# Kernel optimization log

Measured on AMD Instinct MI355X. Metric: run time of the kernel, lower is better.

The kernel has to match this reference:

```python
import jax, jax.numpy as jnp
import numpy as np

D_MODEL = 1024
N_HEADS = 16
D_HEAD = D_MODEL // N_HEADS


def setup_inputs() -> dict:
    key = jax.random.key(0)
    ks = jax.random.split(key, 7)
    x = jax.random.normal(ks[0], (1, 4096, D_MODEL), dtype=jnp.float32)
    # torch Linear default init ~ U(-1/sqrt(fan_in), 1/sqrt(fan_in)); small randn is fine for a reference
    Wqkv = jax.random.normal(ks[1], (3 * D_MODEL, D_MODEL), dtype=jnp.float32) * (1.0 / np.sqrt(D_MODEL))
    bqkv = jax.random.normal(ks[2], (3 * D_MODEL,), dtype=jnp.float32) * 0.01
    Wo = jax.random.normal(ks[3], (D_MODEL, D_MODEL), dtype=jnp.float32) * (1.0 / np.sqrt(D_MODEL))
    bo = jax.random.normal(ks[4], (D_MODEL,), dtype=jnp.float32) * 0.01
    wq = jnp.ones((D_HEAD,), dtype=jnp.float32)
    wk = jnp.ones((D_HEAD,), dtype=jnp.float32)
    return {"x": x, "Wqkv": Wqkv, "bqkv": bqkv, "Wo": Wo, "bo": bo, "wq": wq, "wk": wk}


def _rmsnorm(x, w):
    # matches RMSNormRef: mean of squares over last dim, eps added to mean before sqrt
    xf = x.astype(jnp.float32)
    rms = jnp.mean(xf * xf, axis=-1, keepdims=True)
    return (xf / jnp.sqrt(rms + 1e-6) * w.astype(jnp.float32)).astype(x.dtype)


def reference(x, Wqkv, bqkv, Wo, bo, wq, wk):
    b, s, d = x.shape
    qkv = x @ Wqkv.T + bqkv                       # [b, s, 3d]
    q, k, v = jnp.split(qkv, 3, axis=-1)
    q = q.reshape(b, s, N_HEADS, D_HEAD)
    k = k.reshape(b, s, N_HEADS, D_HEAD)
    v = v.reshape(b, s, N_HEADS, D_HEAD)
    q = _rmsnorm(q, wq)
    k = _rmsnorm(k, wk)
    # NOTE: original applies NO 1/sqrt(d_head) scaling and NO causal mask
    qf = q.astype(jnp.float32)
    kf = k.astype(jnp.float32)
    vf = v.astype(jnp.float32)
    attn = jnp.einsum('bqhd,bkhd->bhqk', qf, kf)  # [b, h, s, s] fp32 scores
    attn = jax.nn.softmax(attn, axis=-1)
    z = jnp.einsum('bhqk,bkhd->bqhd', attn, vf).astype(x.dtype)
    z = z.reshape(b, s, d)
    return z @ Wo.T + bo
```

## Files before the change

### kernel.cpp

```cpp
#include <hip/hip_runtime.h>
#include <hip/hip_bf16.h>

typedef __bf16 bf16;
typedef bf16 bf16x8 __attribute__((ext_vector_type(8)));
typedef bf16 bf16x4 __attribute__((ext_vector_type(4)));
typedef float f32x4 __attribute__((ext_vector_type(4)));
typedef float f32x16 __attribute__((ext_vector_type(16)));
typedef unsigned int u32;
typedef u32 u32x4 __attribute__((ext_vector_type(4)));

static constexpr int SEQ    = 4096;
static constexpr int DMODEL = 1024;
static constexpr int NHEADS = 16;
static constexpr int DHEAD  = 64;
static constexpr int QKV3   = 3 * DMODEL;
static constexpr float SMAX = 64.0f;

__device__ inline void gld16(const bf16* g, bf16* l) {
    __builtin_amdgcn_global_load_lds(
        (const __attribute__((address_space(1))) void*)g,
        (__attribute__((address_space(3))) void*)l, 16, 0, 0);
}

__device__ inline bf16x8 load8(const float* src) {
    float4 a = *(const float4*)(src);
    float4 b = *(const float4*)(src + 4);
    bf16x8 r;
    r[0] = (bf16)a.x; r[1] = (bf16)a.y; r[2] = (bf16)a.z; r[3] = (bf16)a.w;
    r[4] = (bf16)b.x; r[5] = (bf16)b.y; r[6] = (bf16)b.z; r[7] = (bf16)b.w;
    return r;
}

__device__ inline f32x16 zero16() {
    f32x16 r;
#pragma unroll
    for (int i = 0; i < 16; ++i) r[i] = 0.f;
    return r;
}

static constexpr size_t NX = (size_t)SEQ * DMODEL;
static constexpr size_t NW = (size_t)QKV3 * DMODEL;
static constexpr size_t NO = (size_t)DMODEL * DMODEL;

__global__ __launch_bounds__(256)
void cvt_all(const float* __restrict__ x, const float* __restrict__ Wqkv,
             const float* __restrict__ Wo, bf16* __restrict__ outbase) {
    const size_t e = ((size_t)blockIdx.x * 256 + threadIdx.x) * 8;
    const float* src;
    if (e < NX)            src = x + e;
    else if (e < NX + NW)  src = Wqkv + (e - NX);
    else                   src = Wo + (e - NX - NW);
    *(bf16x8*)(outbase + e) = load8(src);
}

__global__ __launch_bounds__(256)
void gemm_qkv(const bf16* __restrict__ A, const bf16* __restrict__ W,
              const float* __restrict__ bias, const float* __restrict__ wq,
              const float* __restrict__ wk, bf16* __restrict__ qkv,
              bf16* __restrict__ Vt) {
    __shared__ __align__(16) bf16 As[128 * 32];
    __shared__ __align__(16) bf16 Ws[128 * 32];
    const int tid  = threadIdx.x;
    const int wave = tid >> 6;
    const int ll   = tid & 15;
    const int quad = (tid & 63) >> 4;
    const int wm   = (wave >> 1) * 64;
    const int wn   = (wave & 1) * 64;
    const int m0 = blockIdx.y * 128;
    const int n0 = blockIdx.x * 128;

    f32x4 acc[4][4];
#pragma unroll
    for (int i = 0; i < 4; ++i)
#pragma unroll
        for (int j = 0; j < 4; ++j) acc[i][j] = (f32x4){0.f, 0.f, 0.f, 0.f};

    for (int k0 = 0; k0 < DMODEL; k0 += 32) {
        __syncthreads();
#pragma unroll
        for (int i = 0; i < 2; ++i) {
            const int idx = i * 256 + tid;
            const int row = idx >> 2;
            const int c   = (idx & 3) ^ ((row >> 1) & 3);
            gld16(&A[(size_t)(m0 + row) * DMODEL + k0 + c * 8], As + idx * 8);
            gld16(&W[(size_t)(n0 + row) * DMODEL + k0 + c * 8], Ws + idx * 8);
        }
        __syncthreads();
        bf16x8 af[4], bfr[4];
#pragma unroll
        for (int mi = 0; mi < 4; ++mi) {
            const int row = wm + mi * 16 + ll;
            af[mi] = *(const bf16x8*)(As + (row * 4 + (quad ^ ((ll >> 1) & 3))) * 8);
        }
#pragma unroll
        for (int ni = 0; ni < 4; ++ni) {
            const int row = wn + ni * 16 + ll;
            bfr[ni] = *(const bf16x8*)(Ws + (row * 4 + (quad ^ ((ll >> 1) & 3))) * 8);
        }
#pragma unroll
        for (int mi = 0; mi < 4; ++mi)
#pragma unroll
            for (int ni = 0; ni < 4; ++ni)
                acc[mi][ni] = __builtin_amdgcn_mfma_f32_16x16x32_bf16(
                    af[mi], bfr[ni], acc[mi][ni], 0, 0, 0);
    }

    float bvn[4];
#pragma unroll
    for (int ni = 0; ni < 4; ++ni) bvn[ni] = bias[n0 + wn + ni * 16 + ll];

    const int sect = (n0 + wn) >> 10;
    if (sect < 2) {
        const float* wv = sect ? wk : wq;
        float wvl[4];
#pragma unroll
        for (int ni = 0; ni < 4; ++ni) wvl[ni] = wv[ni * 16 + ll];
#pragma unroll
        for (int mi = 0; mi < 4; ++mi)
#pragma unroll
            for (int r = 0; r < 4; ++r) {
                float xf[4];
                float ss = 0.f;
#pragma unroll
                for (int ni = 0; ni < 4; ++ni) {
                    xf[ni] = (float)(bf16)(acc[mi][ni][r] + bvn[ni]);
                    ss += xf[ni] * xf[ni];
                }
#pragma unroll
                for (int off = 1; off < 16; off <<= 1) ss += __shfl_xor(ss, off);
                const float scale = rsqrtf(ss * (1.0f / 64.0f) + 1e-6f);
                const int row = m0 + wm + mi * 16 + quad * 4 + r;
#pragma unroll
                for (int ni = 0; ni < 4; ++ni)
                    qkv[(size_t)row * QKV3 + n0 + wn + ni * 16 + ll] =
                        (bf16)(xf[ni] * scale * wvl[ni]);
            }
    } else {
        const int h = (n0 + wn - 2 * DMODEL) >> 6;
#pragma unroll
        for (int mi = 0; mi < 4; ++mi) {
            const int kv = m0 + wm + mi * 16 + quad * 4;
#pragma unroll
            for (int ni = 0; ni < 4; ++ni) {
                bf16x4 vv;
#pragma unroll
                for (int r = 0; r < 4; ++r) vv[r] = (bf16)(acc[mi][ni][r] + bvn[ni]);
                *(bf16x4*)(Vt + (size_t)(h * DHEAD + ni * 16 + ll) * SEQ + kv) = vv;
            }
        }
    }
}

__global__ __launch_bounds__(256)
void gemm_out(const bf16* __restrict__ A, const bf16* __restrict__ W,
              const float* __restrict__ bias, float* __restrict__ C) {
    __shared__ __align__(16) bf16 As[128 * 32];
    __shared__ __align__(16) bf16 Ws[64 * 32];
    const int tid  = threadIdx.x;
    const int wave = tid >> 6;
    const int ll   = tid & 15;
    const int quad = (tid & 63) >> 4;
    const int m0 = blockIdx.y * 128;
    const int n0 = blockIdx.x * 64;

    f32x4 acc[2][4];
#pragma unroll
    for (int i = 0; i < 2; ++i)
#pragma unroll
        for (int j = 0; j < 4; ++j) acc[i][j] = (f32x4){0.f, 0.f, 0.f, 0.f};

    for (int k0 = 0; k0 < DMODEL; k0 += 32) {
        __syncthreads();
#pragma unroll
        for (int i = 0; i < 2; ++i) {
            const int idx = i * 256 + tid;
            const int row = idx >> 2;
            const int c   = (idx & 3) ^ ((row >> 1) & 3);
            gld16(&A[(size_t)(m0 + row) * DMODEL + k0 + c * 8], As + idx * 8);
        }
        {
            const int j   = tid;
            const int row = j >> 2;
            const int c   = (j & 3) ^ ((row >> 1) & 3);
            gld16(&W[(size_t)(n0 + row) * DMODEL + k0 + c * 8], Ws + j * 8);
        }
        __syncthreads();
        bf16x8 af[2], bfr[4];
#pragma unroll
        for (int mi = 0; mi < 2; ++mi) {
            const int row = wave * 32 + mi * 16 + ll;
            af[mi] = *(const bf16x8*)(As + (row * 4 + (quad ^ ((ll >> 1) & 3))) * 8);
        }
#pragma unroll
        for (int ni = 0; ni < 4; ++ni) {
            const int row = ni * 16 + ll;
            bfr[ni] = *(const bf16x8*)(Ws + (row * 4 + (quad ^ ((ll >> 1) & 3))) * 8);
        }
#pragma unroll
        for (int mi = 0; mi < 2; ++mi)
#pragma unroll
            for (int ni = 0; ni < 4; ++ni)
                acc[mi][ni] = __builtin_amdgcn_mfma_f32_16x16x32_bf16(
                    af[mi], bfr[ni], acc[mi][ni], 0, 0, 0);
    }
#pragma unroll
    for (int ni = 0; ni < 4; ++ni) {
        const int col = n0 + ni * 16 + ll;
        const float bv = bias[col];
#pragma unroll
        for (int mi = 0; mi < 2; ++mi)
#pragma unroll
            for (int r = 0; r < 4; ++r) {
                const int row = m0 + wave * 32 + mi * 16 + quad * 4 + r;
                C[(size_t)row * DMODEL + col] = acc[mi][ni][r] + bv;
            }
    }
}

template<bool PARTIAL>
__global__ __launch_bounds__(256, 4)
void attn_fwd(const bf16* __restrict__ qkv, const bf16* __restrict__ Vt,
              bf16* __restrict__ z, float* __restrict__ opf,
              float* __restrict__ lsum) {
    __shared__ __align__(16) bf16 Ks[64 * 64];
    __shared__ __align__(16) bf16 VTs[64 * 64];
    __shared__ __align__(16) float Os[4][32][36];

    const int tid  = threadIdx.x;
    const int wave = tid >> 6;
    const int lane = tid & 63;
    const int l31  = lane & 31;
    const int hh   = lane >> 5;
    const int l7   = lane & 7;
    const int head = blockIdx.x;
    const int q0   = blockIdx.y * 128;
    const int half = PARTIAL ? blockIdx.z : 0;
    const int kvbeg = half * (SEQ / 2);
    const int kvlen = PARTIAL ? (SEQ / 2) : SEQ;

    const bf16* kbase  = qkv + DMODEL + head * DHEAD;
    const bf16* vtbase = Vt + (size_t)head * DHEAD * SEQ;

    bf16* Qs = (bf16*)&Os[0][0][0];
#pragma unroll
    for (int i = 0; i < 4; ++i) {
        const int idx = i * 256 + tid;
        const int row = idx >> 3;
        const int c   = (idx & 7) ^ (row & 7);
        gld16(qkv + (size_t)(q0 + row) * QKV3 + head * DHEAD + c * 8, Qs + idx * 8);
    }
    __syncthreads();
    bf16x8 qf[4];
#pragma unroll
    for (int kd = 0; kd < 4; ++kd)
        qf[kd] = *(const bf16x8*)(Qs + ((wave * 32 + l31) * 8 + ((kd * 2 + hh) ^ l7)) * 8);

    f32x16 o[2];
    o[0] = zero16();
    o[1] = zero16();
    float lp = 0.f;

    for (int kv0 = kvbeg; kv0 < kvbeg + kvlen; kv0 += 64) {
        __syncthreads();
#pragma unroll
        for (int i = 0; i < 2; ++i) {
            const int idx = i * 256 + tid;
            const int row = idx >> 3;
            const int c   = (idx & 7) ^ (row & 7);
            gld16(kbase + (size_t)(kv0 + row) * QKV3 + c * 8, Ks + idx * 8);
            gld16(vtbase + (size_t)row * SEQ + kv0 + c * 8, VTs + idx * 8);
        }
        __syncthreads();

#pragma unroll
        for (int kvt = 0; kvt < 2; ++kvt) {
            f32x16 st = zero16();
#pragma unroll
            for (int kd = 0; kd < 4; ++kd) {
                bf16x8 kf = *(const bf16x8*)(
                    Ks + ((kvt * 32 + l31) * 8 + ((kd * 2 + hh) ^ l7)) * 8);
                st = __builtin_amdgcn_mfma_f32_32x32x16_bf16(kf, qf[kd], st, 0, 0, 0);
            }
            float pf[16];
#pragma unroll
            for (int r = 0; r < 16; ++r) {
                pf[r] = __expf(st[r] - SMAX);
                lp += pf[r];
            }
#pragma unroll
            for (int cc = 0; cc < 2; ++cc) {
                u32 a1, b1, a2, b2;
                asm("v_cvt_pk_bf16_f32 %0, %1, %2" : "=v"(a1) : "v"(pf[8 * cc + 0]), "v"(pf[8 * cc + 1]));
                asm("v_cvt_pk_bf16_f32 %0, %1, %2" : "=v"(b1) : "v"(pf[8 * cc + 4]), "v"(pf[8 * cc + 5]));
                asm("v_cvt_pk_bf16_f32 %0, %1, %2" : "=v"(a2) : "v"(pf[8 * cc + 2]), "v"(pf[8 * cc + 3]));
                asm("v_cvt_pk_bf16_f32 %0, %1, %2" : "=v"(b2) : "v"(pf[8 * cc + 6]), "v"(pf[8 * cc + 7]));
                asm("v_permlane32_swap_b32 %0, %1" : "+v"(a1), "+v"(b1));
                asm("v_permlane32_swap_b32 %0, %1" : "+v"(a2), "+v"(b2));
                u32x4 w;
                w[0] = a1; w[1] = a2; w[2] = b1; w[3] = b2;
                const bf16x8 bp = *(const bf16x8*)&w;
                const int c = kvt * 2 + cc;
#pragma unroll
                for (int dt = 0; dt < 2; ++dt) {
                    bf16x8 vf = *(const bf16x8*)(
                        VTs + ((dt * 32 + l31) * 8 + ((c * 2 + hh) ^ l7)) * 8);
                    o[dt] = __builtin_amdgcn_mfma_f32_32x32x16_bf16(vf, bp, o[dt], 0, 0, 0);
                }
            }
        }
    }

    lp += __shfl_xor(lp, 32);
    const int qrow = q0 + wave * 32 + l31;
    if (PARTIAL) {
        if (lane < 32) lsum[((size_t)half * SEQ + qrow) * NHEADS + head] = lp;
    }
    const float inv = PARTIAL ? 1.0f : 1.0f / lp;

#pragma unroll
    for (int dt = 0; dt < 2; ++dt) {
#pragma unroll
        for (int r = 0; r < 16; ++r) {
            const int dl = (r & 3) + 8 * (r >> 2) + 4 * hh;
            Os[wave][l31][dl] = o[dt][r] * inv;
        }
#pragma unroll
        for (int it = 0; it < 4; ++it) {
            const int qr  = it * 8 + (lane >> 3);
            const int dl2 = (lane & 7) * 4;
            const f32x4 v = *(const f32x4*)(&Os[wave][qr][dl2]);
            const int row = q0 + wave * 32 + qr;
            const int col = head * DHEAD + dt * 32 + dl2;
            if (PARTIAL) {
                *(f32x4*)(opf + ((size_t)half * SEQ + row) * DMODEL + col) = v;
            } else {
                bf16x4 ov;
                ov[0] = (bf16)v[0]; ov[1] = (bf16)v[1];
                ov[2] = (bf16)v[2]; ov[3] = (bf16)v[3];
                *(bf16x4*)(z + (size_t)row * DMODEL + col) = ov;
            }
        }
    }
}

__global__ __launch_bounds__(256)
void combine_halves(const float* __restrict__ opf, const float* __restrict__ lsum,
                    bf16* __restrict__ z) {
    const int row = blockIdx.x;
    const int c   = threadIdx.x * 4;
    const int head = c >> 6;
    const float l = lsum[(size_t)row * NHEADS + head] +
                    lsum[((size_t)SEQ + row) * NHEADS + head];
    const float4 o0 = *(const float4*)(opf + (size_t)row * DMODEL + c);
    const float4 o1 = *(const float4*)(opf + ((size_t)SEQ + row) * DMODEL + c);
    bf16x4 out;
    out[0] = (bf16)((o0.x + o1.x) / l);
    out[1] = (bf16)((o0.y + o1.y) / l);
    out[2] = (bf16)((o0.z + o1.z) / l);
    out[3] = (bf16)((o0.w + o1.w) / l);
    *(bf16x4*)(z + (size_t)row * DMODEL + c) = out;
}

extern "C" void kernel_launch(void* const* d_in, const int* in_sizes, int n_in,
                              void* d_out, int out_size, void* d_ws, size_t ws_size,
                              hipStream_t stream) {
    const float* x    = (const float*)d_in[0];
    const float* Wqkv = (const float*)d_in[1];
    const float* bqkv = (const float*)d_in[2];
    const float* Wo   = (const float*)d_in[3];
    const float* bo   = (const float*)d_in[4];
    const float* wq   = (const float*)d_in[5];
    const float* wk   = (const float*)d_in[6];
    float* out = (float*)d_out;

    bf16* qkv  = (bf16*)d_ws;
    bf16* z    = qkv + (size_t)SEQ * QKV3;
    bf16* Vt   = z + (size_t)SEQ * DMODEL;
    bf16* xb   = Vt + (size_t)NHEADS * DHEAD * SEQ;
    bf16* Wqb  = xb + NX;
    bf16* Wob  = Wqb + NW;
    bf16* endb = Wob + NO;
    float* opf  = (float*)endb;
    float* lsum = opf + (size_t)2 * SEQ * DMODEL;
    const size_t need = (size_t)((char*)(lsum + (size_t)2 * SEQ * NHEADS) - (char*)d_ws);
    const bool split = ws_size >= need;

    cvt_all<<<dim3((NX + NW + NO) / 2048), 256, 0, stream>>>(x, Wqkv, Wo, xb);

    gemm_qkv<<<dim3(QKV3 / 128, SEQ / 128), 256, 0, stream>>>(
        xb, Wqb, bqkv, wq, wk, qkv, Vt);

    if (split) {
        attn_fwd<true><<<dim3(NHEADS, SEQ / 128, 2), 256, 0, stream>>>(
            qkv, Vt, z, opf, lsum);
        combine_halves<<<dim3(SEQ), 256, 0, stream>>>(opf, lsum, z);
    } else {
        attn_fwd<false><<<dim3(NHEADS, SEQ / 128, 1), 256, 0, stream>>>(
            qkv, Vt, z, nullptr, nullptr);
    }

    gemm_out<<<dim3(DMODEL / 64, SEQ / 128), 256, 0, stream>>>(z, Wob, bo, out);
}
```

Measured before the change: 241.4 us.

## Double-buffer K/V tiles in attention and use fused exp2 softmax

Splits the attention K/V shared-memory staging into two buffers, so the next tile's async global-to-LDS load is issued before computing on the current one. This removes one barrier per iteration and overlaps load latency with MFMA work. It also replaces __expf with a single FMA plus exp2 and splits the row-sum into four independent accumulators to shorten the dependency chain. The Q and O staging areas are aliased onto the K/V buffers to keep LDS size bounded, which relies on barrier placement to stay correct.

```diff
diff --git a/kernel.cpp b/kernel.cpp
--- a/kernel.cpp
+++ b/kernel.cpp
@@ -15,6 +15,7 @@
 static constexpr int DHEAD  = 64;
 static constexpr int QKV3   = 3 * DMODEL;
 static constexpr float SMAX = 64.0f;
+static constexpr float LOG2E = 1.44269504088896341f;
 
 __device__ inline void gld16(const bf16* g, bf16* l) {
     __builtin_amdgcn_global_load_lds(
@@ -222,9 +223,9 @@
 void attn_fwd(const bf16* __restrict__ qkv, const bf16* __restrict__ Vt,
               bf16* __restrict__ z, float* __restrict__ opf,
               float* __restrict__ lsum) {
-    __shared__ __align__(16) bf16 Ks[64 * 64];
-    __shared__ __align__(16) bf16 VTs[64 * 64];
-    __shared__ __align__(16) float Os[4][32][36];
+    __shared__ __align__(16) bf16 KV[2][2][64 * 64];
+    float (*Os)[32][36] = (float(*)[32][36])(&KV[0][0][0]);
+    bf16* Qs = &KV[1][0][0];
 
     const int tid  = threadIdx.x;
     const int wave = tid >> 6;
@@ -237,11 +238,22 @@
     const int half = PARTIAL ? blockIdx.z : 0;
     const int kvbeg = half * (SEQ / 2);
     const int kvlen = PARTIAL ? (SEQ / 2) : SEQ;
+    const int nt    = kvlen / 64;
 
     const bf16* kbase  = qkv + DMODEL + head * DHEAD;
     const bf16* vtbase = Vt + (size_t)head * DHEAD * SEQ;
 
-    bf16* Qs = (bf16*)&Os[0][0][0];
+    auto stage_kv = [&](int buf, int kv0) {
+#pragma unroll
+        for (int i = 0; i < 2; ++i) {
+            const int idx = i * 256 + tid;
+            const int row = idx >> 3;
+            const int c   = (idx & 7) ^ (row & 7);
+            gld16(kbase + (size_t)(kv0 + row) * QKV3 + c * 8, &KV[buf][0][0] + idx * 8);
+            gld16(vtbase + (size_t)row * SEQ + kv0 + c * 8, &KV[buf][1][0] + idx * 8);
+        }
+    };
+
 #pragma unroll
     for (int i = 0; i < 4; ++i) {
         const int idx = i * 256 + tid;
@@ -249,28 +261,25 @@
         const int c   = (idx & 7) ^ (row & 7);
         gld16(qkv + (size_t)(q0 + row) * QKV3 + head * DHEAD + c * 8, Qs + idx * 8);
     }
+    stage_kv(0, kvbeg);
     __syncthreads();
+
     bf16x8 qf[4];
 #pragma unroll
     for (int kd = 0; kd < 4; ++kd)
         qf[kd] = *(const bf16x8*)(Qs + ((wave * 32 + l31) * 8 + ((kd * 2 + hh) ^ l7)) * 8);
+    __syncthreads();
 
     f32x16 o[2];
     o[0] = zero16();
     o[1] = zero16();
-    float lp = 0.f;
-
-    for (int kv0 = kvbeg; kv0 < kvbeg + kvlen; kv0 += 64) {
-        __syncthreads();
-#pragma unroll
-        for (int i = 0; i < 2; ++i) {
-            const int idx = i * 256 + tid;
-            const int row = idx >> 3;
-            const int c   = (idx & 7) ^ (row & 7);
-            gld16(kbase + (size_t)(kv0 + row) * QKV3 + c * 8, Ks + idx * 8);
-            gld16(vtbase + (size_t)row * SEQ + kv0 + c * 8, VTs + idx * 8);
-        }
-        __syncthreads();
+    float lpa[4] = {0.f, 0.f, 0.f, 0.f};
+
+    int cur = 0;
+    for (int t = 0; t < nt; ++t) {
+        if (t + 1 < nt) stage_kv(cur ^ 1, kvbeg + (t + 1) * 64);
+        const bf16* Ks  = &KV[cur][0][0];
+        const bf16* VTs = &KV[cur][1][0];
 
 #pragma unroll
         for (int kvt = 0; kvt < 2; ++kvt) {
@@ -283,10 +292,11 @@
             }
             float pf[16];
 #pragma unroll
-            for (int r = 0; r < 16; ++r) {
-                pf[r] = __expf(st[r] - SMAX);
-                lp += pf[r];
-            }
+            for (int r = 0; r < 16; ++r)
+                pf[r] = __builtin_amdgcn_exp2f(
+                    __builtin_fmaf(st[r], LOG2E, -SMAX * LOG2E));
+#pragma unroll
+            for (int r = 0; r < 16; ++r) lpa[r & 3] += pf[r];
 #pragma unroll
             for (int cc = 0; cc < 2; ++cc) {
                 u32 a1, b1, a2, b2;
@@ -308,8 +318,11 @@
                 }
             }
         }
-    }
-
+        __syncthreads();
+        cur ^= 1;
+    }
+
+    float lp = (lpa[0] + lpa[1]) + (lpa[2] + lpa[3]);
     lp += __shfl_xor(lp, 32);
     const int qrow = q0 + wave * 32 + l31;
     if (PARTIAL) {
```

Result: no change. 243.6 us (+0.9%).
